# Performance work log

Hardware: AMD Instinct MI355X
Metric: run time of the kernel (lower is better)

The kernel has to match this reference:

```python
import jax, jax.numpy as jnp
import numpy as np

EMBED_DIM = 256
NUM_HEADS = 8
HEAD_DIM = EMBED_DIM // NUM_HEADS
SCALE = HEAD_DIM ** -0.5  # note: scale uses head_dim even though attention is over full D
EPS = 1e-12  # torch F.normalize eps


def setup_inputs() -> dict:
    key = jax.random.key(0)
    k1, k2, k3 = jax.random.split(key, 3)
    B, Nq, Nk, D = 4, 4096, 4096, EMBED_DIM
    return {
        "query": jax.random.normal(k1, (B, Nq, D), dtype=jnp.float32),
        "key": jax.random.normal(k2, (B, Nk, D), dtype=jnp.float32),
        "value": jax.random.normal(k3, (B, Nk, D), dtype=jnp.float32),
    }


def _l2_normalize(x):
    # matches torch.nn.functional.normalize(x, dim=-1): x / max(||x||, eps)
    n = jnp.linalg.norm(x, axis=-1, keepdims=True)
    return x / jnp.maximum(n, EPS)


def reference(query, key, value):
    q = _l2_normalize(query)          # (B, Nq, D)
    k = _l2_normalize(key)            # (B, Nk, D)
    scores = jnp.einsum("bqd,bkd->bqk", q, k) * SCALE  # (B, Nq, Nk) cosine sims
    attn = jax.nn.softmax(scores, axis=-1)
    return jnp.einsum("bqk,bkd->bqd", attn, value)     # (B, Nq, D)
```

## Files before the change

### kernel.cpp

```cpp
#include <hip/hip_runtime.h>


#define NQ 4096
#define DIM 256
#define NROWS 16384
#define BM 64
#define BN 64
#define KSPLIT 2
#define NITER 32
#define PSTRIDE 68

typedef __attribute__((ext_vector_type(8))) short bf16x8;
typedef __attribute__((ext_vector_type(4))) float f32x4;
typedef __attribute__((ext_vector_type(16))) float f32x16;

__device__ __forceinline__ unsigned short f2bf(float f) {
  unsigned int u = __float_as_uint(f);
  u += 0x7fffu + ((u >> 16) & 1u);
  return (unsigned short)(u >> 16);
}

__device__ __forceinline__ unsigned int pack2bf(float a, float b) {
  unsigned int ua = __float_as_uint(a) + 0x8000u;
  unsigned int ub = __float_as_uint(b) + 0x8000u;
  return __builtin_amdgcn_perm(ub, ua, 0x07060302u);
}

__device__ __forceinline__ void gload16(const void* g, void* l) {
  __builtin_amdgcn_global_load_lds(
      (const __attribute__((address_space(1))) unsigned int*)g,
      (__attribute__((address_space(3))) unsigned int*)l, 16, 0, 0);
}

__device__ __forceinline__ void barrier_lds_only() {
  asm volatile("s_waitcnt lgkmcnt(0)" ::: "memory");
  __builtin_amdgcn_s_barrier();
}

__global__ __launch_bounds__(256) void prep(
    const float* __restrict__ Q, const float* __restrict__ K,
    const float* __restrict__ V,
    unsigned short* __restrict__ Qrm, unsigned short* __restrict__ Kfm,
    unsigned short* __restrict__ Vfm)
{
  __shared__ unsigned short vt[64 * 264];
  const int blk = blockIdx.x, tid = threadIdx.x;
  const int wave = tid >> 6, lane = tid & 63;
  if (blk < 4096) {
    const int R = blk * 4 + wave;
    float4 v = *(const float4*)(Q + (size_t)R * DIM + lane * 4);
    float ss = v.x*v.x + v.y*v.y + v.z*v.z + v.w*v.w;
    #pragma unroll
    for (int off = 1; off < 64; off <<= 1) ss += __shfl_xor(ss, off, 64);
    float scale = (0.17677669529663687f * 1.4426950408889634f)
                  / fmaxf(sqrtf(ss), 1e-12f);
    ushort4 o;
    o.x = f2bf(v.x*scale); o.y = f2bf(v.y*scale);
    o.z = f2bf(v.z*scale); o.w = f2bf(v.w*scale);
    *(ushort4*)(Qrm + (size_t)R * DIM + lane * 4) = o;
  } else if (blk < 4352) {
    const int kt = blk - 4096;
    #pragma unroll
    for (int i = 0; i < 16; i++) {
      const int n = i*4 + wave;
      float4 v = *(const float4*)(K + ((size_t)kt*64 + n) * DIM + lane * 4);
      float ss = v.x*v.x + v.y*v.y + v.z*v.z + v.w*v.w;
      #pragma unroll
      for (int off = 1; off < 64; off <<= 1) ss += __shfl_xor(ss, off, 64);
      float scale = 1.0f / fmaxf(sqrtf(ss), 1e-12f);
      ushort4 o;
      o.x = f2bf(v.x*scale); o.y = f2bf(v.y*scale);
      o.z = f2bf(v.z*scale); o.w = f2bf(v.w*scale);
      *(ushort4*)(vt + n*264 + lane*4) = o;
    }
    __syncthreads();
    #pragma unroll
    for (int s = 0; s < 8; s++) {
      const int ch = tid + 256*s;
      const int c = ch >> 6, n = ch & 63;
      bf16x8 val = *(const bf16x8*)(vt + n*264 + c*8);
      *(bf16x8*)(Kfm + (size_t)kt*16384 + (size_t)ch*8) = val;
    }
  } else {
    const int NS = blk - 4352;
    #pragma unroll
    for (int i = 0; i < 4; i++) {
      const int e = tid + 256*i;
      const int nl = e >> 6, d = (e & 63) * 4;
      float4 v = *(const float4*)(V + ((size_t)NS*16 + nl)*DIM + d);
      ushort4 o;
      o.x = f2bf(v.x); o.y = f2bf(v.y); o.z = f2bf(v.z); o.w = f2bf(v.w);
      *(ushort4*)(vt + nl*264 + d) = o;
    }
    __syncthreads();
    #pragma unroll
    for (int i = 0; i < 2; i++) {
      const int ch = tid + 256*i;
      const int db = ch >> 6, ln = ch & 63;
      const int row0 = (ln >> 5) * 8, dd = db*32 + (ln & 31);
      ushort4 a, b;
      a.x = vt[(row0+0)*264 + dd]; a.y = vt[(row0+1)*264 + dd];
      a.z = vt[(row0+2)*264 + dd]; a.w = vt[(row0+3)*264 + dd];
      b.x = vt[(row0+4)*264 + dd]; b.y = vt[(row0+5)*264 + dd];
      b.z = vt[(row0+6)*264 + dd]; b.w = vt[(row0+7)*264 + dd];
      size_t base = ((size_t)(NS*8 + db)*64 + ln)*8;
      *(ushort4*)(Vfm + base)     = a;
      *(ushort4*)(Vfm + base + 4) = b;
    }
  }
}

__global__ __launch_bounds__(256, 2) void attn(
    const unsigned short* __restrict__ Qrm,
    const unsigned short* __restrict__ Kfm,
    const unsigned short* __restrict__ Vfm,
    float* __restrict__ Opart, float* __restrict__ lpart)
{
  __shared__ unsigned short Klds[2][32 * 64 * 8];
  __shared__ unsigned short Plds[BM * PSTRIDE];

  const int tid = threadIdx.x, wave = tid >> 6, lane = tid & 63;
  const int l15 = lane & 15, l4 = lane >> 4;
  const int blk = blockIdx.x;
  const int g = blk & 7, qt = blk >> 3;
  const int b = g >> 1, ks = g & 1;
  const int Rq0 = b*NQ + qt*BM;
  const int n0base = b*NQ + ks*(NQ/KSPLIT);
  const int mi = wave & 1, ni = wave >> 1;

  bf16x8 qf[2][8];
  #pragma unroll
  for (int mt = 0; mt < 2; mt++) {
    const unsigned short* qrow = Qrm + (size_t)(Rq0 + mi*32 + mt*16 + l15) * DIM + l4*8;
    #pragma unroll
    for (int kg = 0; kg < 8; kg++)
      qf[mt][kg] = *(const bf16x8*)(qrow + kg*32);
  }

  f32x16 oacc[2][2] = {};
  float lacc[2] = {};

  auto stage = [&](int kt, int sel) {
    const unsigned short* src = Kfm + (size_t)((n0base + kt*BN) >> 6) * (32*64*8);
    unsigned short* dst = &Klds[sel][0];
    #pragma unroll
    for (int jj = 0; jj < 4; jj++) {
      const int c = wave*8 + jj*2;
      gload16(src + (size_t)c*512 + lane*8,     dst + (size_t)c*512);
      gload16(src + (size_t)(c+1)*512 + lane*8, dst + (size_t)(c+1)*512);
    }
  };

  stage(0, 0);
  __syncthreads();

  for (int kt = 0; kt < NITER; kt++) {
    if (kt + 1 < NITER) stage(kt + 1, (kt + 1) & 1);

    const unsigned short* kb = &Klds[kt & 1][0];
    f32x4 sacc[2][2] = {};
    #pragma unroll
    for (int kg = 0; kg < 8; kg++) {
      bf16x8 kf[2];
      #pragma unroll
      for (int nt = 0; nt < 2; nt++) {
        const int nrow = ni*32 + nt*16 + l15;
        const int c = kg*4 + l4;
        kf[nt] = *(const bf16x8*)(kb + ((size_t)(c*64 + nrow))*8);
      }
      #pragma unroll
      for (int nt = 0; nt < 2; nt++)
        #pragma unroll
        for (int mt = 0; mt < 2; mt++)
          sacc[nt][mt] = __builtin_amdgcn_mfma_f32_16x16x32_bf16(
              kf[nt], qf[mt][kg], sacc[nt][mt], 0, 0, 0);
    }

    #pragma unroll
    for (int nt = 0; nt < 2; nt++)
      #pragma unroll
      for (int mt = 0; mt < 2; mt++) {
        float p0 = __builtin_amdgcn_exp2f(sacc[nt][mt][0]);
        float p1 = __builtin_amdgcn_exp2f(sacc[nt][mt][1]);
        float p2 = __builtin_amdgcn_exp2f(sacc[nt][mt][2]);
        float p3 = __builtin_amdgcn_exp2f(sacc[nt][mt][3]);
        lacc[mt] += (p0 + p1) + (p2 + p3);
        uint2 pk;
        pk.x = pack2bf(p0, p1);
        pk.y = pack2bf(p2, p3);
        const int m = mi*32 + mt*16 + l15;
        const int n = ni*32 + nt*16 + 4*l4;
        *(uint2*)(Plds + m*PSTRIDE + n) = pk;
      }

    barrier_lds_only();

    const int NB0 = (n0base + kt*BN) >> 4;
    #pragma unroll
    for (int kstep = 0; kstep < 4; kstep++) {
      bf16x8 pf[2], vf[2];
      #pragma unroll
      for (int mt2 = 0; mt2 < 2; mt2++)
        pf[mt2] = *(const bf16x8*)(Plds + (mt2*32 + (lane & 31))*PSTRIDE
                                   + kstep*16 + 8*(lane >> 5));
      #pragma unroll
      for (int dt = 0; dt < 2; dt++) {
        const int db = wave*2 + dt;
        vf[dt] = *(const bf16x8*)(Vfm + ((size_t)((NB0 + kstep)*8 + db)*64 + lane)*8);
      }
      #pragma unroll
      for (int mt2 = 0; mt2 < 2; mt2++)
        #pragma unroll
        for (int dt = 0; dt < 2; dt++)
          oacc[mt2][dt] = __builtin_amdgcn_mfma_f32_32x32x16_bf16(
              pf[mt2], vf[dt], oacc[mt2][dt], 0, 0, 0);
    }

    __syncthreads();
  }

  #pragma unroll
  for (int mt = 0; mt < 2; mt++) {
    float s = lacc[mt];
    s += __shfl_xor(s, 16, 64);
    s += __shfl_xor(s, 32, 64);
    if (l4 == 0)
      lpart[(size_t)(ks*2 + ni)*NROWS + Rq0 + mi*32 + mt*16 + l15] = s;
  }

  #pragma unroll
  for (int mt2 = 0; mt2 < 2; mt2++)
    #pragma unroll
    for (int dt = 0; dt < 2; dt++)
      #pragma unroll
      for (int reg = 0; reg < 16; reg++) {
        const int m = mt2*32 + 4*(lane >> 5) + (reg & 3) + 8*(reg >> 2);
        const int d = wave*64 + dt*32 + (lane & 31);
        Opart[((size_t)(ks*NROWS + Rq0 + m))*DIM + d] = oacc[mt2][dt][reg];
      }
}

__global__ __launch_bounds__(256) void combine(
    const float* __restrict__ Opart, const float* __restrict__ lpart,
    float* __restrict__ out)
{
  const size_t idx = (size_t)blockIdx.x*256 + threadIdx.x;
  const size_t e = idx*4;
  const int R = (int)(e >> 8);
  float4 a = *(const float4*)(Opart + e);
  float4 c = *(const float4*)(Opart + (size_t)NROWS*DIM + e);
  float ls = lpart[R] + lpart[NROWS + R] + lpart[2*NROWS + R] + lpart[3*NROWS + R];
  float inv = 1.0f / ls;
  float4 o;
  o.x = (a.x + c.x)*inv; o.y = (a.y + c.y)*inv;
  o.z = (a.z + c.z)*inv; o.w = (a.w + c.w)*inv;
  *(float4*)(out + e) = o;
}

extern "C" void kernel_launch(void* const* d_in, const int* in_sizes, int n_in,
                              void* d_out, int out_size, void* d_ws, size_t ws_size,
                              hipStream_t stream) {
  const float* Q = (const float*)d_in[0];
  const float* K = (const float*)d_in[1];
  const float* V = (const float*)d_in[2];
  char* ws = (char*)d_ws;
  unsigned short* Qrm = (unsigned short*)(ws);
  unsigned short* Kfm = (unsigned short*)(ws + 8388608);
  unsigned short* Vfm = (unsigned short*)(ws + 16777216);
  float* Opart = (float*)(ws + 25165824);
  float* lpart = (float*)(ws + 58720256);

  prep<<<5376, 256, 0, stream>>>(Q, K, V, Qrm, Kfm, Vfm);
  attn<<<512, 256, 0, stream>>>(Qrm, Kfm, Vfm, Opart, lpart);
  combine<<<4096, 256, 0, stream>>>(Opart, lpart, (float*)d_out);
}
```

Baseline: 188.1 us.

## Split keys four ways, single-buffer K tile, store bf16 partial outputs

Raises the key split from 2 to 4 so the attention kernel launches 1024 blocks, and asks for 4 blocks per CU. The K tile drops from double to single buffering, with the next stage load issued after the P barrier so it overlaps the PV matmul. This frees LDS for the higher occupancy. Partial outputs are stored as bf16 to limit the extra workspace traffic, and combine sums four partials and eight l values. The cost is less load/compute overlap, two full barriers per iteration, and extra rounding of the partial sums.

```diff
diff --git a/kernel.cpp b/kernel.cpp
--- a/kernel.cpp
+++ b/kernel.cpp
@@ -6,8 +6,8 @@
 #define NROWS 16384
 #define BM 64
 #define BN 64
-#define KSPLIT 2
-#define NITER 32
+#define KSPLIT 4
+#define NITER 16
 #define PSTRIDE 68
 
 typedef __attribute__((ext_vector_type(8))) short bf16x8;
@@ -20,6 +20,10 @@
   return (unsigned short)(u >> 16);
 }
 
+__device__ __forceinline__ float bf2f(unsigned short h) {
+  return __uint_as_float((unsigned int)h << 16);
+}
+
 __device__ __forceinline__ unsigned int pack2bf(float a, float b) {
   unsigned int ua = __float_as_uint(a) + 0x8000u;
   unsigned int ub = __float_as_uint(b) + 0x8000u;
@@ -30,11 +34,6 @@
   __builtin_amdgcn_global_load_lds(
       (const __attribute__((address_space(1))) unsigned int*)g,
       (__attribute__((address_space(3))) unsigned int*)l, 16, 0, 0);
-}
-
-__device__ __forceinline__ void barrier_lds_only() {
-  asm volatile("s_waitcnt lgkmcnt(0)" ::: "memory");
-  __builtin_amdgcn_s_barrier();
 }
 
 __global__ __launch_bounds__(256) void prep(
@@ -110,20 +109,20 @@
   }
 }
 
-__global__ __launch_bounds__(256, 2) void attn(
+__global__ __launch_bounds__(256, 4) void attn(
     const unsigned short* __restrict__ Qrm,
     const unsigned short* __restrict__ Kfm,
     const unsigned short* __restrict__ Vfm,
-    float* __restrict__ Opart, float* __restrict__ lpart)
+    unsigned short* __restrict__ Opart, float* __restrict__ lpart)
 {
-  __shared__ unsigned short Klds[2][32 * 64 * 8];
+  __shared__ unsigned short Klds[32 * 64 * 8];
   __shared__ unsigned short Plds[BM * PSTRIDE];
 
   const int tid = threadIdx.x, wave = tid >> 6, lane = tid & 63;
   const int l15 = lane & 15, l4 = lane >> 4;
   const int blk = blockIdx.x;
-  const int g = blk & 7, qt = blk >> 3;
-  const int b = g >> 1, ks = g & 1;
+  const int g = blk & 15, qt = blk >> 4;
+  const int b = g >> 2, ks = g & 3;
   const int Rq0 = b*NQ + qt*BM;
   const int n0base = b*NQ + ks*(NQ/KSPLIT);
   const int mi = wave & 1, ni = wave >> 1;
@@ -140,24 +139,21 @@
   f32x16 oacc[2][2] = {};
   float lacc[2] = {};
 
-  auto stage = [&](int kt, int sel) {
+  auto stage = [&](int kt) {
     const unsigned short* src = Kfm + (size_t)((n0base + kt*BN) >> 6) * (32*64*8);
-    unsigned short* dst = &Klds[sel][0];
     #pragma unroll
     for (int jj = 0; jj < 4; jj++) {
       const int c = wave*8 + jj*2;
-      gload16(src + (size_t)c*512 + lane*8,     dst + (size_t)c*512);
-      gload16(src + (size_t)(c+1)*512 + lane*8, dst + (size_t)(c+1)*512);
+      gload16(src + (size_t)c*512 + lane*8,     Klds + (size_t)c*512);
+      gload16(src + (size_t)(c+1)*512 + lane*8, Klds + (size_t)(c+1)*512);
     }
   };
 
-  stage(0, 0);
-  __syncthreads();
+  stage(0);
 
   for (int kt = 0; kt < NITER; kt++) {
-    if (kt + 1 < NITER) stage(kt + 1, (kt + 1) & 1);
-
-    const unsigned short* kb = &Klds[kt & 1][0];
+    __syncthreads();
+
     f32x4 sacc[2][2] = {};
     #pragma unroll
     for (int kg = 0; kg < 8; kg++) {
@@ -166,7 +162,7 @@
       for (int nt = 0; nt < 2; nt++) {
         const int nrow = ni*32 + nt*16 + l15;
         const int c = kg*4 + l4;
-        kf[nt] = *(const bf16x8*)(kb + ((size_t)(c*64 + nrow))*8);
+        kf[nt] = *(const bf16x8*)(Klds + ((size_t)(c*64 + nrow))*8);
       }
       #pragma unroll
       for (int nt = 0; nt < 2; nt++)
@@ -193,7 +189,9 @@
         *(uint2*)(Plds + m*PSTRIDE + n) = pk;
       }
 
-    barrier_lds_only();
+    __syncthreads();
+
+    if (kt + 1 < NITER) stage(kt + 1);
 
     const int NB0 = (n0base + kt*BN) >> 4;
     #pragma unroll
@@ -215,8 +213,6 @@
           oacc[mt2][dt] = __builtin_amdgcn_mfma_f32_32x32x16_bf16(
               pf[mt2], vf[dt], oacc[mt2][dt], 0, 0, 0);
     }
-
-    __syncthreads();
   }
 
   #pragma unroll
@@ -236,24 +232,30 @@
       for (int reg = 0; reg < 16; reg++) {
         const int m = mt2*32 + 4*(lane >> 5) + (reg & 3) + 8*(reg >> 2);
         const int d = wave*64 + dt*32 + (lane & 31);
-        Opart[((size_t)(ks*NROWS + Rq0 + m))*DIM + d] = oacc[mt2][dt][reg];
+        Opart[((size_t)(ks*NROWS + Rq0 + m))*DIM + d] = f2bf(oacc[mt2][dt][reg]);
       }
 }
 
 __global__ __launch_bounds__(256) void combine(
-    const float* __restrict__ Opart, const float* __restrict__ lpart,
+    const unsigned short* __restrict__ Opart, const float* __restrict__ lpart,
     float* __restrict__ out)
 {
   const size_t idx = (size_t)blockIdx.x*256 + threadIdx.x;
   const size_t e = idx*4;
   const int R = (int)(e >> 8);
-  float4 a = *(const float4*)(Opart + e);
-  float4 c = *(const float4*)(Opart + (size_t)NROWS*DIM + e);
-  float ls = lpart[R] + lpart[NROWS + R] + lpart[2*NROWS + R] + lpart[3*NROWS + R];
+  float acc[4] = {0.f, 0.f, 0.f, 0.f};
+  #pragma unroll
+  for (int s = 0; s < 4; s++) {
+    ushort4 o = *(const ushort4*)(Opart + (size_t)s*NROWS*DIM + e);
+    acc[0] += bf2f(o.x); acc[1] += bf2f(o.y);
+    acc[2] += bf2f(o.z); acc[3] += bf2f(o.w);
+  }
+  float ls = 0.f;
+  #pragma unroll
+  for (int s = 0; s < 8; s++) ls += lpart[(size_t)s*NROWS + R];
   float inv = 1.0f / ls;
   float4 o;
-  o.x = (a.x + c.x)*inv; o.y = (a.y + c.y)*inv;
-  o.z = (a.z + c.z)*inv; o.w = (a.w + c.w)*inv;
+  o.x = acc[0]*inv; o.y = acc[1]*inv; o.z = acc[2]*inv; o.w = acc[3]*inv;
   *(float4*)(out + e) = o;
 }
 
@@ -264,13 +266,13 @@
   const float* K = (const float*)d_in[1];
   const float* V = (const float*)d_in[2];
   char* ws = (char*)d_ws;
-  unsigned short* Qrm = (unsigned short*)(ws);
-  unsigned short* Kfm = (unsigned short*)(ws + 8388608);
-  unsigned short* Vfm = (unsigned short*)(ws + 16777216);
-  float* Opart = (float*)(ws + 25165824);
+  unsigned short* Qrm  = (unsigned short*)(ws);
+  unsigned short* Kfm  = (unsigned short*)(ws + 8388608);
+  unsigned short* Vfm  = (unsigned short*)(ws + 16777216);
+  unsigned short* Opart = (unsigned short*)(ws + 25165824);
   float* lpart = (float*)(ws + 58720256);
 
   prep<<<5376, 256, 0, stream>>>(Q, K, V, Qrm, Kfm, Vfm);
-  attn<<<512, 256, 0, stream>>>(Qrm, Kfm, Vfm, Opart, lpart);
+  attn<<<1024, 256, 0, stream>>>(Qrm, Kfm, Vfm, Opart, lpart);
   combine<<<4096, 256, 0, stream>>>(Opart, lpart, (float*)d_out);
 }
```

Measured after the change: 196.3 us. 1.04x slower.
